# Kernel tuning notes

Hardware: AMD Instinct MI355X
Metric: run time of the kernel (lower is better)

## Reference

```python
import jax, jax.numpy as jnp
import numpy as np

HEADS = 16
DIM_HEAD = 64
SCALE = DIM_HEAD ** -0.5


def setup_inputs() -> dict:
    key = jax.random.key(0)
    k1, k2, k3 = jax.random.split(key, 3)
    B, N, D = 4, 4096, 1024
    inner = HEADS * DIM_HEAD  # 1024
    x = jax.random.normal(k1, (B, N, D), dtype=jnp.float32)
    w_qkv = jax.random.normal(k2, (D, 3 * inner), dtype=jnp.float32) * (D ** -0.5)
    w_out = jax.random.normal(k3, (inner, D), dtype=jnp.float32) * (inner ** -0.5)
    b_out = jnp.zeros((D,), dtype=jnp.float32)
    return {"x": x, "w_qkv": w_qkv, "w_out": w_out, "b_out": b_out}


def reference(x, w_qkv, w_out, b_out):
    B, N, D = x.shape
    inner = HEADS * DIM_HEAD
    qkv = x @ w_qkv  # [B, N, 3*inner]
    q, k, v = jnp.split(qkv, 3, axis=-1)

    def to_heads(t):  # [B, N, inner] -> [B, H, N, Dh]
        return t.reshape(B, N, HEADS, DIM_HEAD).transpose(0, 2, 1, 3)

    q, k, v = to_heads(q), to_heads(k), to_heads(v)
    q = jax.nn.softmax(q * SCALE, axis=-1)   # softmax over feature dim d
    k = jax.nn.softmax(k, axis=-2)           # softmax over sequence dim n
    # context[d, e] = sum_n q[n, d] * k[n, e]
    context = jnp.einsum('bhnd,bhne->bhde', q, k)
    # out[n, e] = sum_d context[d, e] * v[n, d]
    out = jnp.einsum('bhde,bhnd->bhne', context, v)
    out = out.transpose(0, 2, 1, 3).reshape(B, N, inner)  # [B, N, inner]
    return out @ w_out + b_out
```

## Files before the change

kernel.cpp:

```cpp
#include <hip/hip_runtime.h>
#include <hip/hip_bf16.h>

#define SEQ    4096
#define SCALE  0.125f

typedef __attribute__((ext_vector_type(8))) short s8v;
typedef __attribute__((ext_vector_type(4))) float f4v;

__device__ __forceinline__ unsigned short f2bf(float f){
  unsigned int u = __builtin_bit_cast(unsigned int, f);
  u += 0x7FFFu + ((u >> 16) & 1u);
  return (unsigned short)(u >> 16);
}

typedef const __attribute__((address_space(1))) unsigned int gl_uint;
typedef __attribute__((address_space(3))) unsigned int lds_uint;

__device__ __forceinline__ void gload_lds16(const unsigned short* g, unsigned short* l){
  __builtin_amdgcn_global_load_lds((gl_uint*)g, (lds_uint*)l, 16, 0, 0);
}

#define MM(a,b,c) __builtin_amdgcn_mfma_f32_16x16x32_bf16(a,b,c,0,0,0)
#define BAR() __builtin_amdgcn_s_barrier()
#define LGKM0() do{ asm volatile("s_waitcnt lgkmcnt(0)" ::: "memory"); \
                    __builtin_amdgcn_sched_barrier(0); }while(0)
#define VMW(n) asm volatile("s_waitcnt vmcnt(" #n ")" ::: "memory")

__device__ __forceinline__ void mainloop_256(
    const unsigned short* __restrict__ Ag,
    const unsigned short* __restrict__ Bg,
    int bm, int bn, f4v (&acc)[8][4])
{
  __shared__ __align__(16) unsigned short lds[65536];
  const int tid  = threadIdx.x;
  const int wave = tid >> 6, lane = tid & 63;
  const int quad = lane >> 4, l16 = lane & 15;
  const int wmi  = wave >> 2, wni = wave & 3;

  const int schunk = (((tid & 3) ^ ((tid >> 3) & 3)) * 8);
  const unsigned short* aS = Ag + (size_t)(bm + (tid >> 2)) * 1024 + schunk;
  const unsigned short* bS = Bg + (size_t)(bn + (tid >> 2)) * 1024 + schunk;
  unsigned short* ldsw = lds + wave * 512;

  int aoff[8], boff[4];
#pragma unroll
  for (int mf = 0; mf < 8; mf++){
    int r = wmi * 128 + mf * 16 + l16;
    aoff[mf] = r * 32 + ((quad ^ ((r >> 1) & 3)) * 8);
  }
#pragma unroll
  for (int nf = 0; nf < 4; nf++){
    int c = wni * 64 + nf * 16 + l16;
    boff[nf] = 8192 + c * 32 + ((quad ^ ((c >> 1) & 3)) * 8);
  }

#define STG_A(t_) do{ unsigned short* d_ = ldsw + ((t_) & 3) * 16384; \
    const unsigned short* s_ = aS + (t_) * 32; \
    gload_lds16(s_, d_); gload_lds16(s_ + 128 * 1024, d_ + 4096); }while(0)
#define STG_B(t_) do{ unsigned short* d_ = ldsw + ((t_) & 3) * 16384 + 8192; \
    const unsigned short* s_ = bS + (t_) * 32; \
    gload_lds16(s_, d_); gload_lds16(s_ + 128 * 1024, d_ + 4096); }while(0)

  STG_A(0); STG_B(0); STG_A(1); STG_B(1); STG_A(2); STG_B(2);
  VMW(8); BAR();

  s8v a0, a1, a2, a3, b0, b1, b2, b3;

#define PH_A(t_, STG) do{ \
    const unsigned short* base_ = lds + ((t_) & 3) * 16384; \
    b0 = *(const s8v*)(base_ + boff[0]); b1 = *(const s8v*)(base_ + boff[1]); \
    b2 = *(const s8v*)(base_ + boff[2]); b3 = *(const s8v*)(base_ + boff[3]); \
    a0 = *(const s8v*)(base_ + aoff[0]); a1 = *(const s8v*)(base_ + aoff[1]); \
    a2 = *(const s8v*)(base_ + aoff[2]); a3 = *(const s8v*)(base_ + aoff[3]); \
    if (STG) STG_A((t_) + 3); \
    BAR(); LGKM0(); \
    __builtin_amdgcn_s_setprio(1); \
    acc[0][0]=MM(a0,b0,acc[0][0]); acc[0][1]=MM(a0,b1,acc[0][1]); \
    acc[0][2]=MM(a0,b2,acc[0][2]); acc[0][3]=MM(a0,b3,acc[0][3]); \
    acc[1][0]=MM(a1,b0,acc[1][0]); acc[1][1]=MM(a1,b1,acc[1][1]); \
    acc[1][2]=MM(a1,b2,acc[1][2]); acc[1][3]=MM(a1,b3,acc[1][3]); \
    acc[2][0]=MM(a2,b0,acc[2][0]); acc[2][1]=MM(a2,b1,acc[2][1]); \
    acc[2][2]=MM(a2,b2,acc[2][2]); acc[2][3]=MM(a2,b3,acc[2][3]); \
    acc[3][0]=MM(a3,b0,acc[3][0]); acc[3][1]=MM(a3,b1,acc[3][1]); \
    acc[3][2]=MM(a3,b2,acc[3][2]); acc[3][3]=MM(a3,b3,acc[3][3]); \
    __builtin_amdgcn_s_setprio(0); \
    BAR(); }while(0)

#define PH_B(t_, STG, VN) do{ \
    const unsigned short* base_ = lds + ((t_) & 3) * 16384; \
    a0 = *(const s8v*)(base_ + aoff[4]); a1 = *(const s8v*)(base_ + aoff[5]); \
    a2 = *(const s8v*)(base_ + aoff[6]); a3 = *(const s8v*)(base_ + aoff[7]); \
    if (STG) STG_B((t_) + 3); \
    VMW(VN); \
    BAR(); LGKM0(); \
    __builtin_amdgcn_s_setprio(1); \
    acc[4][0]=MM(a0,b0,acc[4][0]); acc[4][1]=MM(a0,b1,acc[4][1]); \
    acc[4][2]=MM(a0,b2,acc[4][2]); acc[4][3]=MM(a0,b3,acc[4][3]); \
    acc[5][0]=MM(a1,b0,acc[5][0]); acc[5][1]=MM(a1,b1,acc[5][1]); \
    acc[5][2]=MM(a1,b2,acc[5][2]); acc[5][3]=MM(a1,b3,acc[5][3]); \
    acc[6][0]=MM(a2,b0,acc[6][0]); acc[6][1]=MM(a2,b1,acc[6][1]); \
    acc[6][2]=MM(a2,b2,acc[6][2]); acc[6][3]=MM(a2,b3,acc[6][3]); \
    acc[7][0]=MM(a3,b0,acc[7][0]); acc[7][1]=MM(a3,b1,acc[7][1]); \
    acc[7][2]=MM(a3,b2,acc[7][2]); acc[7][3]=MM(a3,b3,acc[7][3]); \
    __builtin_amdgcn_s_setprio(0); \
    BAR(); }while(0)

  for (int t = 0; t < 29; ++t){
    PH_A(t, 1);
    PH_B(t, 1, 8);
  }
  PH_A(29, 0); PH_B(29, 0, 4);
  PH_A(30, 0); PH_B(30, 0, 0);
  PH_A(31, 0); PH_B(31, 0, 0);

#undef PH_A
#undef PH_B
#undef STG_A
#undef STG_B
}

__global__ __launch_bounds__(512, 2) void qkv_gemm(
    const unsigned short* __restrict__ A,
    const unsigned short* __restrict__ Bt,
    unsigned short* __restrict__ qt,
    unsigned short* __restrict__ kt,
    unsigned short* __restrict__ vb)
{
  const int id  = blockIdx.x;
  const int swz = (id & 7) * 96 + (id >> 3);
  const int bm  = (swz / 12) * 256, bn = (swz % 12) * 256;

  f4v acc[8][4];
#pragma unroll
  for (int i = 0; i < 8; i++)
#pragma unroll
    for (int j = 0; j < 4; j++) acc[i][j] = (f4v){0.f,0.f,0.f,0.f};

  mainloop_256(A, Bt, bm, bn, acc);

  const int tid = threadIdx.x;
  const int wave = tid >> 6, lane = tid & 63;
  const int quad = lane >> 4, l16 = lane & 15;
  const int wmi = wave >> 2, wni = wave & 3;
  const int colbase = bn + wni * 64;
  const int rowbase = bm + wmi * 128;
  const int sec = colbase >> 10;

  if (sec == 2){
#pragma unroll
    for (int nf = 0; nf < 4; nf++){
      int vc = colbase + nf * 16 + l16 - 2048;
#pragma unroll
      for (int mf = 0; mf < 8; mf++){
        int row = rowbase + mf * 16 + quad * 4;
#pragma unroll
        for (int r = 0; r < 4; r++)
          vb[(size_t)(row + r) * 1024 + vc] = f2bf(acc[mf][nf][r]);
      }
    }
    return;
  }

  if (sec == 0){
#pragma unroll
    for (int mf = 0; mf < 8; mf++){
#pragma unroll
      for (int r = 0; r < 4; r++){
        float m = fmaxf(fmaxf(acc[mf][0][r], acc[mf][1][r]),
                        fmaxf(acc[mf][2][r], acc[mf][3][r]));
        for (int off = 8; off; off >>= 1) m = fmaxf(m, __shfl_xor(m, off));
        m *= SCALE;
        float e0 = __expf(acc[mf][0][r] * SCALE - m);
        float e1 = __expf(acc[mf][1][r] * SCALE - m);
        float e2 = __expf(acc[mf][2][r] * SCALE - m);
        float e3 = __expf(acc[mf][3][r] * SCALE - m);
        float s = (e0 + e1) + (e2 + e3);
        for (int off = 8; off; off >>= 1) s += __shfl_xor(s, off);
        float inv = 1.f / s;
        acc[mf][0][r] = e0 * inv; acc[mf][1][r] = e1 * inv;
        acc[mf][2][r] = e2 * inv; acc[mf][3][r] = e3 * inv;
      }
    }
#pragma unroll
    for (int nf = 0; nf < 4; nf++){
      int col = colbase + nf * 16 + l16;
      int h = (col >> 6) & 15, de = col & 63;
#pragma unroll
      for (int mf = 0; mf < 8; mf++){
        int row = rowbase + mf * 16 + quad * 4;
        int bb = row >> 12, nl = row & 4095;
        ushort4 o;
        o.x = f2bf(acc[mf][nf][0]); o.y = f2bf(acc[mf][nf][1]);
        o.z = f2bf(acc[mf][nf][2]); o.w = f2bf(acc[mf][nf][3]);
        *(ushort4*)&qt[(((size_t)bb * 16 + h) * 64 + de) * SEQ + nl] = o;
      }
    }
  } else {
#pragma unroll
    for (int nf = 0; nf < 4; nf++){
      int col = colbase + nf * 16 + l16;
      int h = (col >> 6) & 15, de = col & 63;
#pragma unroll
      for (int mf = 0; mf < 8; mf++){
        int row = rowbase + mf * 16 + quad * 4;
        int bb = row >> 12, nl = row & 4095;
        ushort4 o;
        o.x = f2bf(__expf(acc[mf][nf][0])); o.y = f2bf(__expf(acc[mf][nf][1]));
        o.z = f2bf(__expf(acc[mf][nf][2])); o.w = f2bf(__expf(acc[mf][nf][3]));
        *(ushort4*)&kt[(((size_t)bb * 16 + h) * 64 + de) * SEQ + nl] = o;
      }
    }
  }
}

__global__ __launch_bounds__(512, 2) void gemm_final(
    const unsigned short* __restrict__ A,
    const unsigned short* __restrict__ C2t,
    float* __restrict__ Cf,
    const float* __restrict__ bias)
{
  const int id  = blockIdx.x;
  const int swz = (id & 7) * 32 + (id >> 3);
  const int bm  = (swz >> 2) * 256, bn = (swz & 3) * 256;
  const unsigned short* Bt = C2t + (size_t)(bm >> 12) * 1024 * 1024;

  f4v acc[8][4];
#pragma unroll
  for (int i = 0; i < 8; i++)
#pragma unroll
    for (int j = 0; j < 4; j++) acc[i][j] = (f4v){0.f,0.f,0.f,0.f};

  mainloop_256(A, Bt, bm, bn, acc);

  const int tid = threadIdx.x;
  const int wave = tid >> 6, lane = tid & 63;
  const int quad = lane >> 4, l16 = lane & 15;
  const int wmi = wave >> 2, wni = wave & 3;

#pragma unroll
  for (int nf = 0; nf < 4; nf++){
    int col = bn + wni * 64 + nf * 16 + l16;
    float bv = bias[col];
#pragma unroll
    for (int mf = 0; mf < 8; mf++){
      int row = bm + wmi * 128 + mf * 16 + quad * 4;
#pragma unroll
      for (int r = 0; r < 4; r++)
        Cf[(size_t)(row + r) * 1024 + col] = acc[mf][nf][r] + bv;
    }
  }
}

__global__ void cvt_f32_bf16(const float4* __restrict__ in, ushort4* __restrict__ outp){
  int i = blockIdx.x * 256 + threadIdx.x;
  float4 v = in[i];
  ushort4 o;
  o.x = f2bf(v.x); o.y = f2bf(v.y); o.z = f2bf(v.z); o.w = f2bf(v.w);
  outp[i] = o;
}

__global__ __launch_bounds__(256) void transpose_cvt(const float* __restrict__ in,
                                                     unsigned short* __restrict__ outp,
                                                     int R, int C){
  __shared__ float tile[64][65];
  int r0 = blockIdx.y * 64, c0 = blockIdx.x * 64;
  int t = threadIdx.x;
  for (int i = t; i < 4096; i += 256){ int r = i >> 6, c = i & 63;
    tile[r][c] = in[(size_t)(r0 + r) * C + c0 + c]; }
  __syncthreads();
  for (int i = t; i < 4096; i += 256){ int c = i >> 6, r = i & 63;
    outp[(size_t)(c0 + c) * R + r0 + r] = f2bf(tile[r][c]); }
}

__global__ __launch_bounds__(256) void ctx_partial(const unsigned short* __restrict__ qt,
                                                   const unsigned short* __restrict__ kt,
                                                   float* __restrict__ ctxp){
  __shared__ float red[4096];
  int bh = blockIdx.x >> 2, ch = blockIdx.x & 3;
  int t = threadIdx.x, wave = t >> 6, lane = t & 63, quad = lane >> 4, l16 = lane & 15;
  const unsigned short* qb = qt + (size_t)bh * 64 * SEQ;
  const unsigned short* kb = kt + (size_t)bh * 64 * SEQ;
  f4v acc[4][4];
#pragma unroll
  for (int i = 0; i < 4; i++)
#pragma unroll
    for (int j = 0; j < 4; j++) acc[i][j] = (f4v){0.f,0.f,0.f,0.f};
  int ns = ch * 1024 + wave * 256;
  for (int n0 = ns; n0 < ns + 256; n0 += 32){
    s8v af[4], bf[4];
#pragma unroll
    for (int mt = 0; mt < 4; mt++) af[mt] = *(const s8v*)&qb[(size_t)(mt*16 + l16) * SEQ + n0 + quad*8];
#pragma unroll
    for (int nt = 0; nt < 4; nt++) bf[nt] = *(const s8v*)&kb[(size_t)(nt*16 + l16) * SEQ + n0 + quad*8];
#pragma unroll
    for (int mt = 0; mt < 4; mt++)
#pragma unroll
      for (int nt = 0; nt < 4; nt++)
        acc[mt][nt] = __builtin_amdgcn_mfma_f32_16x16x32_bf16(af[mt], bf[nt], acc[mt][nt], 0, 0, 0);
  }
  for (int i = t; i < 4096; i += 256) red[i] = 0.f;
  __syncthreads();
  for (int w = 0; w < 4; w++){
    if (wave == w){
#pragma unroll
      for (int mt = 0; mt < 4; mt++)
#pragma unroll
        for (int nt = 0; nt < 4; nt++)
#pragma unroll
          for (int r = 0; r < 4; r++)
            red[(mt*16 + quad*4 + r) * 64 + nt*16 + l16] += acc[mt][nt][r];
    }
    __syncthreads();
  }
  float* cp = ctxp + (size_t)blockIdx.x * 4096;
  for (int i = t; i < 4096; i += 256) cp[i] = red[i];
}

__global__ __launch_bounds__(256) void ctx2_kernel(const float* __restrict__ ctxp,
                                                   const float* __restrict__ w_out,
                                                   unsigned short* __restrict__ ctx2t){
  __shared__ float ctxs[4096];
  __shared__ float inv_s[64];
  int bh = blockIdx.x >> 4, fc = blockIdx.x & 15;
  int b = bh >> 4, h = bh & 15;
  int t = threadIdx.x;
  int fl = t & 63, dg = t >> 6;
  int f = fc * 64 + fl;
  for (int i = t; i < 4096; i += 256){
    const float* p = ctxp + (size_t)bh * 4 * 4096 + i;
    ctxs[i] = (p[0] + p[4096]) + (p[8192] + p[12288]);
  }
  __syncthreads();
  if (t < 64){
    float s = 0.f;
#pragma unroll
    for (int d = 0; d < 64; d++) s += ctxs[d * 64 + t];
    inv_s[t] = 1.f / s;
  }
  __syncthreads();
  float acc[16];
#pragma unroll
  for (int i = 0; i < 16; i++) acc[i] = 0.f;
  for (int e = 0; e < 64; e++){
    float w = w_out[(size_t)(h * 64 + e) * 1024 + f] * inv_s[e];
#pragma unroll
    for (int dd = 0; dd < 16; dd++)
      acc[dd] += ctxs[(dg * 16 + dd) * 64 + e] * w;
  }
  unsigned short* op = ctx2t + ((size_t)b * 1024 + f) * 1024 + h * 64 + dg * 16;
#pragma unroll
  for (int g = 0; g < 4; g++){
    ushort4 o;
    o.x = f2bf(acc[g*4+0]); o.y = f2bf(acc[g*4+1]);
    o.z = f2bf(acc[g*4+2]); o.w = f2bf(acc[g*4+3]);
    *(ushort4*)&op[g*4] = o;
  }
}

extern "C" void kernel_launch(void* const* d_in, const int* in_sizes, int n_in,
                              void* d_out, int out_size, void* d_ws, size_t ws_size,
                              hipStream_t stream) {
  const float* x     = (const float*)d_in[0];
  const float* w_qkv = (const float*)d_in[1];
  const float* w_out = (const float*)d_in[2];
  const float* b_out = (const float*)d_in[3];
  float* out = (float*)d_out;

  const int M = 4 * SEQ;

  unsigned short* xb = (unsigned short*)d_out;

  char* wp = (char*)d_ws;
  size_t off = 0;
  auto nxt = [&](size_t bytes) -> char* {
    char* p = wp + off;
    off += (bytes + 255) & ~(size_t)255;
    return p;
  };
  unsigned short* wqkvT = (unsigned short*)nxt((size_t)3072 * 1024 * 2);
  unsigned short* qt    = (unsigned short*)nxt((size_t)64 * 64 * SEQ * 2);
  unsigned short* kt    = (unsigned short*)nxt((size_t)64 * 64 * SEQ * 2);
  unsigned short* vb    = (unsigned short*)nxt((size_t)M * 1024 * 2);
  float*          ctxp  = (float*)wqkvT;
  unsigned short* ctx2t = qt;

  cvt_f32_bf16<<<(M * 1024) / 4 / 256, 256, 0, stream>>>((const float4*)x, (ushort4*)xb);
  transpose_cvt<<<dim3(3072 / 64, 1024 / 64), 256, 0, stream>>>(w_qkv, wqkvT, 1024, 3072);

  qkv_gemm<<<768, 512, 0, stream>>>(xb, wqkvT, qt, kt, vb);

  ctx_partial<<<64 * 4, 256, 0, stream>>>(qt, kt, ctxp);

  ctx2_kernel<<<64 * 16, 256, 0, stream>>>(ctxp, w_out, ctx2t);

  gemm_final<<<256, 512, 0, stream>>>(vb, ctx2t, out, b_out);
}
```

Measured before the change: 343.9 us.

## Software-pipeline LDS fragment loads with double-buffered registers in QKV GEMM mainloop

Restructures the 256x256 GEMM mainloop so each iteration prefetches the next k-tile's A/B fragments from LDS into a second register set while MFMAs run on the current set. This cuts the barriers per k-step from four to one and drops the explicit lgkmcnt waits. Per-fragment offset arrays are replaced with a single base plus constant strides, which assumes the swizzle term is independent of the fragment index. The cost is roughly double the fragment registers, which may pressure occupancy at launch_bounds(512,2). It also changes the vmcnt wait pattern, with a risk of LDS buffer reuse hazards.

Result: no change. 349.1 us (+1.5%).

```diff
diff --git a/kernel.cpp b/kernel.cpp
--- a/kernel.cpp
+++ b/kernel.cpp
@@ -22,9 +22,21 @@
 
 #define MM(a,b,c) __builtin_amdgcn_mfma_f32_16x16x32_bf16(a,b,c,0,0,0)
 #define BAR() __builtin_amdgcn_s_barrier()
-#define LGKM0() do{ asm volatile("s_waitcnt lgkmcnt(0)" ::: "memory"); \
-                    __builtin_amdgcn_sched_barrier(0); }while(0)
+#define SB0() __builtin_amdgcn_sched_barrier(0)
 #define VMW(n) asm volatile("s_waitcnt vmcnt(" #n ")" ::: "memory")
+
+__device__ __forceinline__ void mfmaH0(const s8v (&A)[8], const s8v (&B)[4], f4v (&acc)[8][4]){
+#pragma unroll
+  for (int m = 0; m < 4; m++)
+#pragma unroll
+    for (int n = 0; n < 4; n++) acc[m][n] = MM(A[m], B[n], acc[m][n]);
+}
+__device__ __forceinline__ void mfmaH1(const s8v (&A)[8], const s8v (&B)[4], f4v (&acc)[8][4]){
+#pragma unroll
+  for (int m = 4; m < 8; m++)
+#pragma unroll
+    for (int n = 0; n < 4; n++) acc[m][n] = MM(A[m], B[n], acc[m][n]);
+}
 
 __device__ __forceinline__ void mainloop_256(
     const unsigned short* __restrict__ Ag,
@@ -36,23 +48,16 @@
   const int wave = tid >> 6, lane = tid & 63;
   const int quad = lane >> 4, l16 = lane & 15;
   const int wmi  = wave >> 2, wni = wave & 3;
+  const char* ldsc = (const char*)lds;
+
+  const int c16   = (quad ^ ((l16 >> 1) & 3)) * 16;
+  const int abase = (wmi * 128 + l16) * 64 + c16;
+  const int bbase = 16384 + (wni * 64 + l16) * 64 + c16;
 
   const int schunk = (((tid & 3) ^ ((tid >> 3) & 3)) * 8);
   const unsigned short* aS = Ag + (size_t)(bm + (tid >> 2)) * 1024 + schunk;
   const unsigned short* bS = Bg + (size_t)(bn + (tid >> 2)) * 1024 + schunk;
   unsigned short* ldsw = lds + wave * 512;
-
-  int aoff[8], boff[4];
-#pragma unroll
-  for (int mf = 0; mf < 8; mf++){
-    int r = wmi * 128 + mf * 16 + l16;
-    aoff[mf] = r * 32 + ((quad ^ ((r >> 1) & 3)) * 8);
-  }
-#pragma unroll
-  for (int nf = 0; nf < 4; nf++){
-    int c = wni * 64 + nf * 16 + l16;
-    boff[nf] = 8192 + c * 32 + ((quad ^ ((c >> 1) & 3)) * 8);
-  }
 
 #define STG_A(t_) do{ unsigned short* d_ = ldsw + ((t_) & 3) * 16384; \
     const unsigned short* s_ = aS + (t_) * 32; \
@@ -61,60 +66,47 @@
     const unsigned short* s_ = bS + (t_) * 32; \
     gload_lds16(s_, d_); gload_lds16(s_ + 128 * 1024, d_ + 4096); }while(0)
 
+#define LD_B4(NB, base_) do{ \
+    NB[0] = *(const s8v*)((base_) + bbase);        NB[1] = *(const s8v*)((base_) + bbase + 1024); \
+    NB[2] = *(const s8v*)((base_) + bbase + 2048); NB[3] = *(const s8v*)((base_) + bbase + 3072); }while(0)
+#define LD_A4LO(NA, base_) do{ \
+    NA[0] = *(const s8v*)((base_) + abase);        NA[1] = *(const s8v*)((base_) + abase + 1024); \
+    NA[2] = *(const s8v*)((base_) + abase + 2048); NA[3] = *(const s8v*)((base_) + abase + 3072); }while(0)
+#define LD_A4HI(NA, base_) do{ \
+    NA[4] = *(const s8v*)((base_) + abase + 4096); NA[5] = *(const s8v*)((base_) + abase + 5120); \
+    NA[6] = *(const s8v*)((base_) + abase + 6144); NA[7] = *(const s8v*)((base_) + abase + 7168); }while(0)
+
+  s8v A0[8], B0[4], A1[8], B1[4];
+
   STG_A(0); STG_B(0); STG_A(1); STG_B(1); STG_A(2); STG_B(2);
   VMW(8); BAR();
-
-  s8v a0, a1, a2, a3, b0, b1, b2, b3;
-
-#define PH_A(t_, STG) do{ \
-    const unsigned short* base_ = lds + ((t_) & 3) * 16384; \
-    b0 = *(const s8v*)(base_ + boff[0]); b1 = *(const s8v*)(base_ + boff[1]); \
-    b2 = *(const s8v*)(base_ + boff[2]); b3 = *(const s8v*)(base_ + boff[3]); \
-    a0 = *(const s8v*)(base_ + aoff[0]); a1 = *(const s8v*)(base_ + aoff[1]); \
-    a2 = *(const s8v*)(base_ + aoff[2]); a3 = *(const s8v*)(base_ + aoff[3]); \
-    if (STG) STG_A((t_) + 3); \
-    BAR(); LGKM0(); \
-    __builtin_amdgcn_s_setprio(1); \
-    acc[0][0]=MM(a0,b0,acc[0][0]); acc[0][1]=MM(a0,b1,acc[0][1]); \
-    acc[0][2]=MM(a0,b2,acc[0][2]); acc[0][3]=MM(a0,b3,acc[0][3]); \
-    acc[1][0]=MM(a1,b0,acc[1][0]); acc[1][1]=MM(a1,b1,acc[1][1]); \
-    acc[1][2]=MM(a1,b2,acc[1][2]); acc[1][3]=MM(a1,b3,acc[1][3]); \
-    acc[2][0]=MM(a2,b0,acc[2][0]); acc[2][1]=MM(a2,b1,acc[2][1]); \
-    acc[2][2]=MM(a2,b2,acc[2][2]); acc[2][3]=MM(a2,b3,acc[2][3]); \
-    acc[3][0]=MM(a3,b0,acc[3][0]); acc[3][1]=MM(a3,b1,acc[3][1]); \
-    acc[3][2]=MM(a3,b2,acc[3][2]); acc[3][3]=MM(a3,b3,acc[3][3]); \
-    __builtin_amdgcn_s_setprio(0); \
-    BAR(); }while(0)
-
-#define PH_B(t_, STG, VN) do{ \
-    const unsigned short* base_ = lds + ((t_) & 3) * 16384; \
-    a0 = *(const s8v*)(base_ + aoff[4]); a1 = *(const s8v*)(base_ + aoff[5]); \
-    a2 = *(const s8v*)(base_ + aoff[6]); a3 = *(const s8v*)(base_ + aoff[7]); \
-    if (STG) STG_B((t_) + 3); \
-    VMW(VN); \
-    BAR(); LGKM0(); \
-    __builtin_amdgcn_s_setprio(1); \
-    acc[4][0]=MM(a0,b0,acc[4][0]); acc[4][1]=MM(a0,b1,acc[4][1]); \
-    acc[4][2]=MM(a0,b2,acc[4][2]); acc[4][3]=MM(a0,b3,acc[4][3]); \
-    acc[5][0]=MM(a1,b0,acc[5][0]); acc[5][1]=MM(a1,b1,acc[5][1]); \
-    acc[5][2]=MM(a1,b2,acc[5][2]); acc[5][3]=MM(a1,b3,acc[5][3]); \
-    acc[6][0]=MM(a2,b0,acc[6][0]); acc[6][1]=MM(a2,b1,acc[6][1]); \
-    acc[6][2]=MM(a2,b2,acc[6][2]); acc[6][3]=MM(a2,b3,acc[6][3]); \
-    acc[7][0]=MM(a3,b0,acc[7][0]); acc[7][1]=MM(a3,b1,acc[7][1]); \
-    acc[7][2]=MM(a3,b2,acc[7][2]); acc[7][3]=MM(a3,b3,acc[7][3]); \
-    __builtin_amdgcn_s_setprio(0); \
-    BAR(); }while(0)
-
-  for (int t = 0; t < 29; ++t){
-    PH_A(t, 1);
-    PH_B(t, 1, 8);
-  }
-  PH_A(29, 0); PH_B(29, 0, 4);
-  PH_A(30, 0); PH_B(30, 0, 0);
-  PH_A(31, 0); PH_B(31, 0, 0);
-
-#undef PH_A
-#undef PH_B
+  LD_B4(B0, ldsc); LD_A4LO(A0, ldsc); LD_A4HI(A0, ldsc);
+
+#define BODY(T_, CA, CB, NA, NB, DOSTG, VMWx) do{ \
+    VMWx; BAR(); SB0(); \
+    if (DOSTG){ STG_A((T_) + 3); STG_B((T_) + 3); } \
+    { const char* nb_ = ldsc + ((((T_) + 1) & 3) << 15); \
+      LD_B4(NB, nb_); LD_A4LO(NA, nb_); \
+      __builtin_amdgcn_s_setprio(1); mfmaH0(CA, CB, acc); __builtin_amdgcn_s_setprio(0); \
+      LD_A4HI(NA, nb_); \
+      __builtin_amdgcn_s_setprio(1); mfmaH1(CA, CB, acc); __builtin_amdgcn_s_setprio(0); } \
+  }while(0)
+
+  for (int t = 0; t < 28; t += 2){
+    BODY(t,     A0, B0, A1, B1, 1, VMW(4));
+    BODY(t + 1, A1, B1, A0, B0, 1, VMW(4));
+  }
+  BODY(28, A0, B0, A1, B1, 1, VMW(4));
+  BODY(29, A1, B1, A0, B0, 0, VMW(4));
+  BODY(30, A0, B0, A1, B1, 0, VMW(0));
+  __builtin_amdgcn_s_setprio(1);
+  mfmaH0(A1, B1, acc); mfmaH1(A1, B1, acc);
+  __builtin_amdgcn_s_setprio(0);
+
+#undef BODY
+#undef LD_B4
+#undef LD_A4LO
+#undef LD_A4HI
 #undef STG_A
 #undef STG_B
 }
```
